# Kernel optimization log

Hardware: AMD Instinct MI355X
Metric: run time of the kernel (lower is better)

## Reference

```python
import jax, jax.numpy as jnp
import numpy as np

B, P = 4, 50000
D_IN, COND = 3, 48
# layer l: in IN_DIMS[l] -> out OUT_DIMS[l]; dims=[3,256*8,257], skip at layer index 4
IN_DIMS  = [D_IN + COND, 256, 256, 256, 256, 256, 256, 256, 256]
OUT_DIMS = [256, 256, 256, 253, 256, 256, 256, 256, 257]
N_LIN = 9
INV_SQRT2 = np.float32(1.0 / np.sqrt(2.0))


def softplus_beta100(x):
    return jax.nn.softplus(100.0 * x) * 0.01


def setup_inputs() -> dict:
    key = jax.random.key(0)
    ks = jax.random.split(key, 2 + 2 * N_LIN)
    inp = {
        "input": jax.random.normal(ks[0], (B, P, D_IN), dtype=jnp.float32),
        "cond_pose": jax.random.normal(ks[1], (B, COND), dtype=jnp.float32),
    }
    for l in range(N_LIN):
        scale = np.float32(np.sqrt(2.0 / OUT_DIMS[l]))  # geometry-style init scale
        inp[f"W{l}"] = jax.random.normal(ks[2 + 2 * l], (OUT_DIMS[l], IN_DIMS[l]), dtype=jnp.float32) * scale
        inp[f"b{l}"] = jnp.zeros((OUT_DIMS[l],), dtype=jnp.float32)
    return inp


def reference(input, cond_pose,
              W0, b0, W1, b1, W2, b2, W3, b3, W4, b4, W5, b5, W6, b6, W7, b7, W8, b8):
    Ws = [W0, W1, W2, W3, W4, W5, W6, W7, W8]
    bs = [b0, b1, b2, b3, b4, b5, b6, b7, b8]
    nb, npnt, nd = input.shape
    x_in = input.reshape(nb * npnt, nd)                                   # (N, 3)
    c = jnp.broadcast_to(cond_pose[:, None, :], (nb, npnt, COND)).reshape(nb * npnt, COND)
    x = jnp.concatenate([x_in, c], axis=-1)                               # cond concat at layer 0
    for l in range(N_LIN):
        if l == 4:  # skip connection: concat raw input, scaled by 1/sqrt(2)
            x = jnp.concatenate([x, x_in], axis=-1) * INV_SQRT2
        x = x @ Ws[l].T + bs[l]
        if l < N_LIN - 1:
            x = softplus_beta100(x)
    return x.reshape(nb, npnt, -1)                                        # (B, P, 257)
```

## Files before the change

### kernel.cpp

```cpp
#include <hip/hip_runtime.h>


typedef __attribute__((ext_vector_type(8))) short bf16x8;
typedef __attribute__((ext_vector_type(4))) float f32x4;
typedef __attribute__((ext_vector_type(2))) float f32x2;

#define PPTS 50000

__device__ __forceinline__ short f2bf(float f) {
    union { float f; unsigned u; } v; v.f = f;
    unsigned r = v.u + 0x7fffu + ((v.u >> 16) & 1u);
    return (short)(r >> 16);
}

__device__ __forceinline__ unsigned cvt_pk_bf16(float lo, float hi) {
    unsigned r;
    asm("v_cvt_pk_bf16_f32 %0, %1, %2" : "=v"(r) : "v"(lo), "v"(hi));
    return r;
}

__device__ __forceinline__ void bar_lgkm() {
    asm volatile("s_waitcnt lgkmcnt(0)" ::: "memory");
    __builtin_amdgcn_s_barrier();
    __builtin_amdgcn_sched_barrier(0);
}

__device__ __forceinline__ f32x2 sp100_pair(f32x2 y) {
    const f32x2 A2 = {6.9314718e-3f, 6.9314718e-3f};
    const f32x2 B2 = {-3.11522e-3f, -3.11522e-3f};
    const f32x2 C2 = {9.8829e-4f,  9.8829e-4f};
    const f32x2 K2 = {-144.26950408889634f, -144.26950408889634f};
    const f32x2 Z2 = {0.0f, 0.0f};
    f32x2 m = __builtin_elementwise_abs(y) * K2;
    f32x2 e = {__builtin_amdgcn_exp2f(m.x), __builtin_amdgcn_exp2f(m.y)};
    f32x2 t = __builtin_elementwise_fma(C2, e, B2);
    t = __builtin_elementwise_fma(t, e, A2);
    return __builtin_elementwise_fma(e, t, __builtin_elementwise_max(y, Z2));
}
__device__ __forceinline__ void sp100_4(f32x4& v) {
    f32x2 y0 = {v[0], v[1]}, y1 = {v[2], v[3]};
    f32x2 r0 = sp100_pair(y0), r1 = sp100_pair(y1);
    v[0] = r0.x; v[1] = r0.y; v[2] = r1.x; v[3] = r1.y;
}

__device__ __forceinline__ int xswz(int row) {
    return (((row & 7) ^ (5 * ((row >> 3) & 1))) << 4);
}
__device__ __forceinline__ short* xaddr(short* base, int row, int col) {
    int off = ((row << 9) + (col << 1)) ^ xswz(row);
    return (short*)((char*)base + off);
}
__device__ __forceinline__ const short* xaddrc(const short* base, int row, int col) {
    int off = ((row << 9) + (col << 1)) ^ xswz(row);
    return (const short*)((const char*)base + off);
}

__global__ void prep_kernel(
    const float* __restrict__ W0, const float* __restrict__ W1, const float* __restrict__ W2,
    const float* __restrict__ W3, const float* __restrict__ W4, const float* __restrict__ W5,
    const float* __restrict__ W6, const float* __restrict__ W7, const float* __restrict__ W8,
    short* __restrict__ wbf)
{
    const int gid = blockIdx.x * blockDim.x + threadIdx.x;
    if (gid >= 68096) return;
    int l, cid; const float* Wsrc;
    if      (gid <  2048) { l = 0; cid = gid;         Wsrc = W0; }
    else if (gid < 10240) { l = 1; cid = gid -  2048; Wsrc = W1; }
    else if (gid < 18432) { l = 2; cid = gid - 10240; Wsrc = W2; }
    else if (gid < 26624) { l = 3; cid = gid - 18432; Wsrc = W3; }
    else if (gid < 34816) { l = 4; cid = gid - 26624; Wsrc = W4; }
    else if (gid < 43008) { l = 5; cid = gid - 34816; Wsrc = W5; }
    else if (gid < 51200) { l = 6; cid = gid - 43008; Wsrc = W6; }
    else if (gid < 59392) { l = 7; cid = gid - 51200; Wsrc = W7; }
    else                  { l = 8; cid = gid - 59392; Wsrc = W8; }
    const int NR   = (l == 3) ? 253 : ((l == 8) ? 257 : 256);
    const int KR   = (l == 0) ? 51 : 256;
    const int klog = (l == 0) ? 1 : 3;
    const float sc = (l == 4) ? 0.70710678f : 1.0f;
    const int lane  = cid & 63;
    const int tile  = cid >> 6;
    const int ntile = tile >> klog;
    const int ktile = tile & ((1 << klog) - 1);
    const int n  = ntile * 16 + (lane & 15);
    const int k0 = ktile * 32 + ((lane >> 4) << 3);
    bf16x8 v;
#pragma unroll
    for (int j = 0; j < 8; ++j) {
        int k = k0 + j;
        float f = (n < NR && k < KR) ? Wsrc[n * KR + k] * sc : 0.0f;
        v[j] = f2bf(f);
    }
    ((bf16x8*)wbf)[gid] = v;
}

template<int KSTEPS, int MODE, int MODE_NEXT>
__device__ __forceinline__ void layer_fwd(const short* src, short* dst,
    const bf16x8* __restrict__ wl, const bf16x8* __restrict__ wlnext,
    const float* __restrict__ bias_next, int lane, int wid,
    bf16x8 (&ap)[4], f32x4 (&bp)[4])
{
    const int prow = lane & 15;
    const int kg   = (lane >> 4) << 3;
    const int rb4  = (lane >> 4) << 2;
    f32x4 acc[4][4];
#pragma unroll
    for (int nii = 0; nii < 4; ++nii)
#pragma unroll
        for (int mi = 0; mi < 4; ++mi)
            acc[mi][nii] = bp[nii];
    bf16x8 a_cur[4], b_cur[4];
#pragma unroll
    for (int nii = 0; nii < 4; ++nii) a_cur[nii] = ap[nii];
#pragma unroll
    for (int mi = 0; mi < 4; ++mi)
        b_cur[mi] = *(const bf16x8*)xaddrc(src, mi * 16 + prow, kg);
#pragma unroll
    for (int ks = 0; ks < KSTEPS; ++ks) {
        bf16x8 a_nxt[4], b_nxt[4];
        if (ks + 1 < KSTEPS) {
#pragma unroll
            for (int nii = 0; nii < 4; ++nii)
                a_nxt[nii] = wl[((wid * 4 + nii) * KSTEPS + ks + 1) * 64 + lane];
#pragma unroll
            for (int mi = 0; mi < 4; ++mi)
                b_nxt[mi] = *(const bf16x8*)xaddrc(src, mi * 16 + prow,
                                                   (ks + 1) * 32 + kg);
        } else {
#pragma unroll
            for (int nii = 0; nii < 4; ++nii)
                a_nxt[nii] = wlnext[(wid * 4 + nii) * 512 + lane];
        }
        __builtin_amdgcn_s_setprio(1);
#pragma unroll
        for (int mi = 0; mi < 4; ++mi)
#pragma unroll
            for (int nii = 0; nii < 4; ++nii)
                acc[mi][nii] = __builtin_amdgcn_mfma_f32_16x16x32_bf16(
                    a_cur[nii], b_cur[mi], acc[mi][nii], 0, 0, 0);
        __builtin_amdgcn_s_setprio(0);
#pragma unroll
        for (int nii = 0; nii < 4; ++nii) a_cur[nii] = a_nxt[nii];
        if (ks + 1 < KSTEPS) {
#pragma unroll
            for (int mi = 0; mi < 4; ++mi) b_cur[mi] = b_nxt[mi];
        }
    }
#pragma unroll
    for (int nii = 0; nii < 4; ++nii) ap[nii] = a_cur[nii];
#pragma unroll
    for (int nii = 0; nii < 4; ++nii) {
        const int cb = (wid * 4 + nii) * 16 + rb4;
        if (MODE_NEXT == 1 && cb == 252) {
            f32x4 tb = {bias_next[252], 0.f, 0.f, 0.f}; bp[nii] = tb;
        } else {
            bp[nii] = *(const f32x4*)(bias_next + cb);
        }
    }
#pragma unroll
    for (int nii = 0; nii < 4; ++nii)
#pragma unroll
        for (int mi = 0; mi < 4; ++mi)
            sp100_4(acc[mi][nii]);
#pragma unroll
    for (int nii = 0; nii < 4; ++nii) {
        const int cb = (wid * 4 + nii) * 16 + rb4;
#pragma unroll
        for (int mi = 0; mi < 4; ++mi) {
            unsigned p01 = cvt_pk_bf16(acc[mi][nii][0], acc[mi][nii][1]);
            unsigned p23 = cvt_pk_bf16(acc[mi][nii][2], acc[mi][nii][3]);
            if (MODE == 1 && cb == 252) {
                *xaddr(dst, mi * 16 + prow, 252) = (short)(p01 & 0xffff);
            } else {
                uint2 pk; pk.x = p01; pk.y = p23;
                *(uint2*)xaddr(dst, mi * 16 + prow, cb) = pk;
            }
        }
    }
}

__global__ __launch_bounds__(256, 2) void net_kernel(
    const float* __restrict__ xin, const float* __restrict__ cond,
    const bf16x8* __restrict__ W,
    const float* __restrict__ b0, const float* __restrict__ b1, const float* __restrict__ b2,
    const float* __restrict__ b3, const float* __restrict__ b4, const float* __restrict__ b5,
    const float* __restrict__ b6, const float* __restrict__ b7, const float* __restrict__ b8,
    float* __restrict__ out)
{
    __shared__ short xb0[64 * 256];
    __shared__ short xb1[64 * 256];
    const int t    = threadIdx.x;
    const int pt0  = blockIdx.x * 64;
    const int lane = t & 63;
    const int wid  = t >> 6;
    const int rb4  = (lane >> 4) << 2;

    bf16x8 ap[4];
    f32x4  bp[4];
#pragma unroll
    for (int nii = 0; nii < 4; ++nii) {
        ap[nii] = W[(wid * 4 + nii) * 128 + lane];
        bp[nii] = *(const f32x4*)(b0 + (wid * 4 + nii) * 16 + rb4);
    }

    float sk[3] = {0.f, 0.f, 0.f};
    if (t < 64) {
#pragma unroll
        for (int c = 0; c < 3; ++c)
            sk[c] = xin[(pt0 + t) * 3 + c];
    }

    {
        const int row   = t >> 2;
        const int c0    = (t & 3) << 4;
        const int point = pt0 + row;
        const int batch = point / PPTS;
        const float* xp = xin + point * 3;
        const float* cp = cond + batch * 48;
#pragma unroll
        for (int h = 0; h < 2; ++h) {
            bf16x8 v;
#pragma unroll
            for (int i = 0; i < 8; ++i) {
                int c = c0 + h * 8 + i;
                float f = (c < 3) ? xp[c] : ((c < 51) ? cp[c - 3] : 0.0f);
                v[i] = f2bf(f);
            }
            *(bf16x8*)xaddr(xb0, row, c0 + h * 8) = v;
        }
    }
    bar_lgkm();

    layer_fwd<2, 0, 0>(xb0, xb1, W +     0, W +  2048, b1, lane, wid, ap, bp); bar_lgkm();
    layer_fwd<8, 0, 0>(xb1, xb0, W +  2048, W + 10240, b2, lane, wid, ap, bp); bar_lgkm();
    layer_fwd<8, 0, 1>(xb0, xb1, W + 10240, W + 18432, b3, lane, wid, ap, bp); bar_lgkm();
    if (t < 64) {
#pragma unroll
        for (int c = 0; c < 3; ++c)
            *xaddr(xb0, t, 253 + c) = f2bf(sk[c]);
    }
    layer_fwd<8, 1, 0>(xb1, xb0, W + 18432, W + 26624, b4, lane, wid, ap, bp); bar_lgkm();
    layer_fwd<8, 0, 0>(xb0, xb1, W + 26624, W + 34816, b5, lane, wid, ap, bp); bar_lgkm();
    layer_fwd<8, 0, 0>(xb1, xb0, W + 34816, W + 43008, b6, lane, wid, ap, bp); bar_lgkm();
    layer_fwd<8, 0, 0>(xb0, xb1, W + 43008, W + 51200, b7, lane, wid, ap, bp); bar_lgkm();
    layer_fwd<8, 0, 0>(xb1, xb0, W + 51200, W + 59392, b8, lane, wid, ap, bp); bar_lgkm();

    {
        const bf16x8* wl = W + 59392;
        const int prow = lane & 15;
        const int kg   = (lane >> 4) << 3;
        const float blast = b8[256];
#pragma unroll
        for (int half = 0; half < 2; ++half) {
            f32x4 acc[2][4];
            f32x4 acc2[2];
#pragma unroll
            for (int nii = 0; nii < 4; ++nii) {
#pragma unroll
                for (int m2 = 0; m2 < 2; ++m2)
                    acc[m2][nii] = bp[nii];
            }
            {
                f32x4 bz = {(rb4 == 0) ? blast : 0.f, 0.f, 0.f, 0.f};
                acc2[0] = bz; acc2[1] = bz;
            }
            bf16x8 a_cur[4];
#pragma unroll
            for (int nii = 0; nii < 4; ++nii)
                a_cur[nii] = (half == 0) ? ap[nii]
                           : wl[((wid * 4 + nii) * 8) * 64 + lane];
#pragma unroll
            for (int ks = 0; ks < 8; ++ks) {
                bf16x8 a_nxt[4], a2;
                if (ks < 7) {
#pragma unroll
                    for (int nii = 0; nii < 4; ++nii)
                        a_nxt[nii] = wl[((wid * 4 + nii) * 8 + ks + 1) * 64 + lane];
                }
                if (wid == 0) a2 = wl[(128 + ks) * 64 + lane];
                bf16x8 b[2];
#pragma unroll
                for (int m2 = 0; m2 < 2; ++m2)
                    b[m2] = *(const bf16x8*)xaddrc(xb0, (half * 2 + m2) * 16 + prow,
                                                   ks * 32 + kg);
                __builtin_amdgcn_s_setprio(1);
#pragma unroll
                for (int m2 = 0; m2 < 2; ++m2)
#pragma unroll
                    for (int nii = 0; nii < 4; ++nii)
                        acc[m2][nii] = __builtin_amdgcn_mfma_f32_16x16x32_bf16(
                            a_cur[nii], b[m2], acc[m2][nii], 0, 0, 0);
                if (wid == 0) {
#pragma unroll
                    for (int m2 = 0; m2 < 2; ++m2)
                        acc2[m2] = __builtin_amdgcn_mfma_f32_16x16x32_bf16(
                            a2, b[m2], acc2[m2], 0, 0, 0);
                }
                __builtin_amdgcn_s_setprio(0);
                if (ks < 7) {
#pragma unroll
                    for (int nii = 0; nii < 4; ++nii) a_cur[nii] = a_nxt[nii];
                }
            }
#pragma unroll
            for (int nii = 0; nii < 4; ++nii) {
                const int cb = (wid * 4 + nii) * 16 + rb4;
#pragma unroll
                for (int m2 = 0; m2 < 2; ++m2) {
                    const int rowoff = (pt0 + (half * 2 + m2) * 16 + prow) * 257 + cb;
#pragma unroll
                    for (int r = 0; r < 4; ++r)
                        out[rowoff + r] = acc[m2][nii][r];
                }
            }
            if (wid == 0 && rb4 == 0) {
#pragma unroll
                for (int m2 = 0; m2 < 2; ++m2)
                    out[(pt0 + (half * 2 + m2) * 16 + prow) * 257 + 256]
                        = acc2[m2][0];
            }
        }
    }
}

extern "C" void kernel_launch(void* const* d_in, const int* in_sizes, int n_in,
                              void* d_out, int out_size, void* d_ws, size_t ws_size,
                              hipStream_t stream)
{
    const float* xin  = (const float*)d_in[0];
    const float* cond = (const float*)d_in[1];
    const float* Wp[9]; const float* bp[9];
    for (int l = 0; l < 9; ++l) { Wp[l] = (const float*)d_in[2 + 2 * l]; bp[l] = (const float*)d_in[3 + 2 * l]; }
    short* wbf = (short*)d_ws;

    prep_kernel<<<dim3(266), dim3(256), 0, stream>>>(
        Wp[0], Wp[1], Wp[2], Wp[3], Wp[4], Wp[5], Wp[6], Wp[7], Wp[8], wbf);
    net_kernel<<<dim3(3125), dim3(256), 0, stream>>>(
        xin, cond, (const bf16x8*)wbf,
        bp[0], bp[1], bp[2], bp[3], bp[4], bp[5], bp[6], bp[7], bp[8],
        (float*)d_out);
}
```

Baseline: 279.5 us.

## Split output columns across 8 waves per block and drop register prefetch

Each block now runs 512 threads (8 waves) over the same 64-point tile, and each wave owns 2 N-tiles (32 output columns) instead of 4. Register double-buffering of weight and activation fragments is removed in favour of direct loads per k-step, with the next layer's first weight fragment fetched after the loop. The intent is to cut per-thread register pressure so more waves fit per CU (launch bounds 512,4), hiding latency through occupancy rather than software prefetch. In exchange each wave gets less MFMA work per activation LDS read, so LDS traffic per FLOP rises, and barriers now synchronise twice as many waves.

```diff
diff --git a/kernel.cpp b/kernel.cpp
--- a/kernel.cpp
+++ b/kernel.cpp
@@ -97,59 +97,47 @@
 __device__ __forceinline__ void layer_fwd(const short* src, short* dst,
     const bf16x8* __restrict__ wl, const bf16x8* __restrict__ wlnext,
     const float* __restrict__ bias_next, int lane, int wid,
-    bf16x8 (&ap)[4], f32x4 (&bp)[4])
+    bf16x8 (&ap)[2], f32x4 (&bp)[2])
 {
     const int prow = lane & 15;
     const int kg   = (lane >> 4) << 3;
     const int rb4  = (lane >> 4) << 2;
-    f32x4 acc[4][4];
-#pragma unroll
-    for (int nii = 0; nii < 4; ++nii)
+    f32x4 acc[4][2];
+#pragma unroll
+    for (int nii = 0; nii < 2; ++nii)
 #pragma unroll
         for (int mi = 0; mi < 4; ++mi)
             acc[mi][nii] = bp[nii];
-    bf16x8 a_cur[4], b_cur[4];
-#pragma unroll
-    for (int nii = 0; nii < 4; ++nii) a_cur[nii] = ap[nii];
-#pragma unroll
-    for (int mi = 0; mi < 4; ++mi)
-        b_cur[mi] = *(const bf16x8*)xaddrc(src, mi * 16 + prow, kg);
 #pragma unroll
     for (int ks = 0; ks < KSTEPS; ++ks) {
-        bf16x8 a_nxt[4], b_nxt[4];
-        if (ks + 1 < KSTEPS) {
-#pragma unroll
-            for (int nii = 0; nii < 4; ++nii)
-                a_nxt[nii] = wl[((wid * 4 + nii) * KSTEPS + ks + 1) * 64 + lane];
-#pragma unroll
-            for (int mi = 0; mi < 4; ++mi)
-                b_nxt[mi] = *(const bf16x8*)xaddrc(src, mi * 16 + prow,
-                                                   (ks + 1) * 32 + kg);
-        } else {
-#pragma unroll
-            for (int nii = 0; nii < 4; ++nii)
-                a_nxt[nii] = wlnext[(wid * 4 + nii) * 512 + lane];
-        }
-        __builtin_amdgcn_s_setprio(1);
-#pragma unroll
-        for (int mi = 0; mi < 4; ++mi)
-#pragma unroll
-            for (int nii = 0; nii < 4; ++nii)
-                acc[mi][nii] = __builtin_amdgcn_mfma_f32_16x16x32_bf16(
-                    a_cur[nii], b_cur[mi], acc[mi][nii], 0, 0, 0);
-        __builtin_amdgcn_s_setprio(0);
-#pragma unroll
-        for (int nii = 0; nii < 4; ++nii) a_cur[nii] = a_nxt[nii];
-        if (ks + 1 < KSTEPS) {
-#pragma unroll
-            for (int mi = 0; mi < 4; ++mi) b_cur[mi] = b_nxt[mi];
-        }
-    }
-#pragma unroll
-    for (int nii = 0; nii < 4; ++nii) ap[nii] = a_cur[nii];
-#pragma unroll
-    for (int nii = 0; nii < 4; ++nii) {
-        const int cb = (wid * 4 + nii) * 16 + rb4;
+        bf16x8 a[2];
+#pragma unroll
+        for (int nii = 0; nii < 2; ++nii)
+            a[nii] = (ks == 0) ? ap[nii]
+                   : wl[((wid * 2 + nii) * KSTEPS + ks) * 64 + lane];
+#pragma unroll
+        for (int mh = 0; mh < 2; ++mh) {
+            bf16x8 b[2];
+#pragma unroll
+            for (int m2 = 0; m2 < 2; ++m2)
+                b[m2] = *(const bf16x8*)xaddrc(src, (mh * 2 + m2) * 16 + prow,
+                                               ks * 32 + kg);
+            __builtin_amdgcn_s_setprio(1);
+#pragma unroll
+            for (int m2 = 0; m2 < 2; ++m2)
+#pragma unroll
+                for (int nii = 0; nii < 2; ++nii)
+                    acc[mh * 2 + m2][nii] = __builtin_amdgcn_mfma_f32_16x16x32_bf16(
+                        a[nii], b[m2], acc[mh * 2 + m2][nii], 0, 0, 0);
+            __builtin_amdgcn_s_setprio(0);
+        }
+    }
+#pragma unroll
+    for (int nii = 0; nii < 2; ++nii)
+        ap[nii] = wlnext[(wid * 2 + nii) * 512 + lane];
+#pragma unroll
+    for (int nii = 0; nii < 2; ++nii) {
+        const int cb = (wid * 2 + nii) * 16 + rb4;
         if (MODE_NEXT == 1 && cb == 252) {
             f32x4 tb = {bias_next[252], 0.f, 0.f, 0.f}; bp[nii] = tb;
         } else {
@@ -157,13 +145,13 @@
         }
     }
 #pragma unroll
-    for (int nii = 0; nii < 4; ++nii)
+    for (int nii = 0; nii < 2; ++nii)
 #pragma unroll
         for (int mi = 0; mi < 4; ++mi)
             sp100_4(acc[mi][nii]);
 #pragma unroll
-    for (int nii = 0; nii < 4; ++nii) {
-        const int cb = (wid * 4 + nii) * 16 + rb4;
+    for (int nii = 0; nii < 2; ++nii) {
+        const int cb = (wid * 2 + nii) * 16 + rb4;
 #pragma unroll
         for (int mi = 0; mi < 4; ++mi) {
             unsigned p01 = cvt_pk_bf16(acc[mi][nii][0], acc[mi][nii][1]);
@@ -178,7 +166,7 @@
     }
 }
 
-__global__ __launch_bounds__(256, 2) void net_kernel(
+__global__ __launch_bounds__(512, 4) void net_kernel(
     const float* __restrict__ xin, const float* __restrict__ cond,
     const bf16x8* __restrict__ W,
     const float* __restrict__ b0, const float* __restrict__ b1, const float* __restrict__ b2,
@@ -194,12 +182,12 @@
     const int wid  = t >> 6;
     const int rb4  = (lane >> 4) << 2;
 
-    bf16x8 ap[4];
-    f32x4  bp[4];
-#pragma unroll
-    for (int nii = 0; nii < 4; ++nii) {
-        ap[nii] = W[(wid * 4 + nii) * 128 + lane];
-        bp[nii] = *(const f32x4*)(b0 + (wid * 4 + nii) * 16 + rb4);
+    bf16x8 ap[2];
+    f32x4  bp[2];
+#pragma unroll
+    for (int nii = 0; nii < 2; ++nii) {
+        ap[nii] = W[(wid * 2 + nii) * 128 + lane];
+        bp[nii] = *(const f32x4*)(b0 + (wid * 2 + nii) * 16 + rb4);
     }
 
     float sk[3] = {0.f, 0.f, 0.f};
@@ -210,23 +198,20 @@
     }
 
     {
-        const int row   = t >> 2;
-        const int c0    = (t & 3) << 4;
+        const int row   = t >> 3;
+        const int c0    = (t & 7) << 3;
         const int point = pt0 + row;
         const int batch = point / PPTS;
         const float* xp = xin + point * 3;
         const float* cp = cond + batch * 48;
-#pragma unroll
-        for (int h = 0; h < 2; ++h) {
-            bf16x8 v;
-#pragma unroll
-            for (int i = 0; i < 8; ++i) {
-                int c = c0 + h * 8 + i;
-                float f = (c < 3) ? xp[c] : ((c < 51) ? cp[c - 3] : 0.0f);
-                v[i] = f2bf(f);
-            }
-            *(bf16x8*)xaddr(xb0, row, c0 + h * 8) = v;
-        }
+        bf16x8 v;
+#pragma unroll
+        for (int i = 0; i < 8; ++i) {
+            int c = c0 + i;
+            float f = (c < 3) ? xp[c] : ((c < 51) ? cp[c - 3] : 0.0f);
+            v[i] = f2bf(f);
+        }
+        *(bf16x8*)xaddr(xb0, row, c0) = v;
     }
     bar_lgkm();
 
@@ -251,31 +236,24 @@
         const float blast = b8[256];
 #pragma unroll
         for (int half = 0; half < 2; ++half) {
-            f32x4 acc[2][4];
+            f32x4 acc[2][2];
             f32x4 acc2[2];
 #pragma unroll
-            for (int nii = 0; nii < 4; ++nii) {
+            for (int nii = 0; nii < 2; ++nii)
 #pragma unroll
                 for (int m2 = 0; m2 < 2; ++m2)
                     acc[m2][nii] = bp[nii];
-            }
             {
                 f32x4 bz = {(rb4 == 0) ? blast : 0.f, 0.f, 0.f, 0.f};
                 acc2[0] = bz; acc2[1] = bz;
             }
-            bf16x8 a_cur[4];
-#pragma unroll
-            for (int nii = 0; nii < 4; ++nii)
-                a_cur[nii] = (half == 0) ? ap[nii]
-                           : wl[((wid * 4 + nii) * 8) * 64 + lane];
 #pragma unroll
             for (int ks = 0; ks < 8; ++ks) {
-                bf16x8 a_nxt[4], a2;
-                if (ks < 7) {
-#pragma unroll
-                    for (int nii = 0; nii < 4; ++nii)
-                        a_nxt[nii] = wl[((wid * 4 + nii) * 8 + ks + 1) * 64 + lane];
-                }
+                bf16x8 a[2], a2;
+#pragma unroll
+                for (int nii = 0; nii < 2; ++nii)
+                    a[nii] = (half == 0 && ks == 0) ? ap[nii]
+                           : wl[((wid * 2 + nii) * 8 + ks) * 64 + lane];
                 if (wid == 0) a2 = wl[(128 + ks) * 64 + lane];
                 bf16x8 b[2];
 #pragma unroll
@@ -286,9 +264,9 @@
 #pragma unroll
                 for (int m2 = 0; m2 < 2; ++m2)
 #pragma unroll
-                    for (int nii = 0; nii < 4; ++nii)
+                    for (int nii = 0; nii < 2; ++nii)
                         acc[m2][nii] = __builtin_amdgcn_mfma_f32_16x16x32_bf16(
-                            a_cur[nii], b[m2], acc[m2][nii], 0, 0, 0);
+                            a[nii], b[m2], acc[m2][nii], 0, 0, 0);
                 if (wid == 0) {
 #pragma unroll
                     for (int m2 = 0; m2 < 2; ++m2)
@@ -296,14 +274,10 @@
                             a2, b[m2], acc2[m2], 0, 0, 0);
                 }
                 __builtin_amdgcn_s_setprio(0);
-                if (ks < 7) {
-#pragma unroll
-                    for (int nii = 0; nii < 4; ++nii) a_cur[nii] = a_nxt[nii];
-                }
-            }
-#pragma unroll
-            for (int nii = 0; nii < 4; ++nii) {
-                const int cb = (wid * 4 + nii) * 16 + rb4;
+            }
+#pragma unroll
+            for (int nii = 0; nii < 2; ++nii) {
+                const int cb = (wid * 2 + nii) * 16 + rb4;
 #pragma unroll
                 for (int m2 = 0; m2 < 2; ++m2) {
                     const int rowoff = (pt0 + (half * 2 + m2) * 16 + prow) * 257 + cb;
@@ -334,7 +308,7 @@
 
     prep_kernel<<<dim3(266), dim3(256), 0, stream>>>(
         Wp[0], Wp[1], Wp[2], Wp[3], Wp[4], Wp[5], Wp[6], Wp[7], Wp[8], wbf);
-    net_kernel<<<dim3(3125), dim3(256), 0, stream>>>(
+    net_kernel<<<dim3(3125), dim3(512), 0, stream>>>(
         xin, cond, (const bf16x8*)wbf,
         bp[0], bp[1], bp[2], bp[3], bp[4], bp[5], bp[6], bp[7], bp[8],
         (float*)d_out);
```

Measured after the change: 299.9 us. 7.3% more time.
